# Kernel tuning notes

Hardware: AMD Instinct MI355X
Metric: run time of the kernel (lower is better)

Reference implementation:

```python
import jax, jax.numpy as jnp
import numpy as np

B = 4
N_CPGS = 20000
N_FREQS = N_CPGS // 2 + 1  # rfft length
E = 320000
H = 4
HD = 16          # head_dim = graph_hidden // n_heads
GH = 64          # graph_hidden
FD = 64          # fusion_dim
FH = 128         # fft_hidden
PH = 128         # plasticity_hidden


def _ln(x, g, b, eps=1e-5):
    m = x.mean(-1, keepdims=True)
    v = ((x - m) ** 2).mean(-1, keepdims=True)
    return (x - m) / jnp.sqrt(v + eps) * g + b


def _gelu(x):
    return jax.nn.gelu(x, approximate=False)  # torch default: exact erf GELU


def setup_inputs() -> dict:
    key = jax.random.key(0)
    ki = iter(jax.random.split(key, 40))
    nrm = lambda shape, s=0.02: jax.random.normal(next(ki), shape, dtype=jnp.float32) * s
    z = lambda *s: jnp.zeros(s, jnp.float32)
    o = lambda *s: jnp.ones(s, jnp.float32)
    return dict(
        x=jax.random.uniform(next(ki), (B, N_CPGS), dtype=jnp.float32),
        edge_index=jax.random.randint(next(ki), (2, E), 0, N_CPGS, dtype=jnp.int32),
        fft_freq_weights=o(N_FREQS),
        fft_w1=nrm((FH, N_FREQS)), fft_b1=z(FH), fft_ln1_g=o(FH), fft_ln1_b=z(FH),
        fft_w2=nrm((FD, FH)), fft_b2=z(FD), fft_ln2_g=o(FD), fft_ln2_b=z(FD),
        ge_w=nrm((GH, 1)), ge_b=z(GH), ge_ln_g=o(GH), ge_ln_b=z(GH),
        gat_w=nrm((GH, GH)), gat_attn=nrm((H, 2 * HD), 0.1),
        gp_w=nrm((FD, GH)), gp_b=z(FD), gp_ln_g=o(FD), gp_ln_b=z(FD),
        pl_W=nrm((PH, N_FREQS), 0.01), pl_alpha=o(PH, N_FREQS) * 0.01,
        pl_eta=jnp.array([0.1], jnp.float32), pl_bias=z(PH),
        pn_g=o(PH), pn_b=z(PH),
        pp_w=nrm((FD, PH)), pp_b=z(FD), pp_ln_g=o(FD), pp_ln_b=z(FD),
        gate_w1=nrm((6, 3 * FD)), gate_b1=z(6), gate_w2=nrm((3, 6)), gate_b2=z(3),
        head_w1=nrm((32, FD)), head_b1=z(32), head_w2=nrm((1, 32)), head_b2=z(1),
    )


def reference(x, edge_index, fft_freq_weights,
              fft_w1, fft_b1, fft_ln1_g, fft_ln1_b, fft_w2, fft_b2, fft_ln2_g, fft_ln2_b,
              ge_w, ge_b, ge_ln_g, ge_ln_b, gat_w, gat_attn,
              gp_w, gp_b, gp_ln_g, gp_ln_b,
              pl_W, pl_alpha, pl_eta, pl_bias, pn_g, pn_b,
              pp_w, pp_b, pp_ln_g, pp_ln_b,
              gate_w1, gate_b1, gate_w2, gate_b2,
              head_w1, head_b1, head_w2, head_b2):
    Bsz, n = x.shape
    # ---- Stream 1: FFT ----
    xc = x - x.mean(axis=1, keepdims=True)
    mag = jnp.log1p(jnp.abs(jnp.fft.rfft(xc, axis=1)))          # (B, N_FREQS)
    freq_w = jax.nn.softmax(fft_freq_weights) * fft_freq_weights.shape[0]
    magw = mag * freq_w[None, :]
    f = _gelu(_ln(magw @ fft_w1.T + fft_b1, fft_ln1_g, fft_ln1_b))
    fft_feat = _ln(f @ fft_w2.T + fft_b2, fft_ln2_g, fft_ln2_b)  # (B, FD)
    # ---- Stream 2: sparse graph attention (eval: dropout off) ----
    h0 = _gelu(_ln(x[..., None] * ge_w[:, 0] + ge_b, ge_ln_g, ge_ln_b))  # (B, N, GH)
    h = (h0 @ gat_w.T).reshape(Bsz, n, H, HD)
    a_src, a_dst = gat_attn[:, :HD], gat_attn[:, HD:]
    s_src = jnp.einsum('bnhd,hd->bnh', h, a_src)
    s_dst = jnp.einsum('bnhd,hd->bnh', h, a_dst)
    src, dst = edge_index[0], edge_index[1]
    scores = s_src[:, src] + s_dst[:, dst]                       # (B, E, H)
    scores = jnp.where(scores >= 0, scores, 0.2 * scores)        # leaky_relu(0.2)
    # max with include_self=True over zero-init buffer (matches torch scatter_reduce)
    m = jnp.zeros((Bsz, n, H), scores.dtype).at[:, dst].max(scores)
    e = jnp.exp(scores - m[:, dst])
    ssum = jnp.zeros((Bsz, n, H), e.dtype).at[:, dst].add(e)
    attn = e / (ssum[:, dst] + 1e-8)
    msg = h[:, src] * attn[..., None]                            # (B, E, H, HD)
    gat_out = jnp.zeros((Bsz, n, H, HD), msg.dtype).at[:, dst].add(msg).reshape(Bsz, n, H * HD)
    hg = h0 + _gelu(gat_out)
    graph_feat = _ln(hg.mean(axis=1) @ gp_w.T + gp_b, gp_ln_g, gp_ln_b)  # (B, FD)
    # ---- Stream 3: Hebbian plastic layer on mag ----
    y_slow = mag @ pl_W.T + pl_bias                              # (B, PH)
    x_norm = mag / (jnp.linalg.norm(mag, axis=-1, keepdims=True) + 1e-8)
    y_pre = jnp.tanh(y_slow)
    # bmm(alpha * eta * outer(y_pre, x_norm), x) == eta * y_pre * ((x_norm*x) @ alpha.T)
    contrib = pl_eta[0] * y_pre * ((x_norm * mag) @ jax.nn.sigmoid(pl_alpha).T)
    plastic = _ln(_gelu(y_slow + contrib), pn_g, pn_b)
    plastic_feat = _ln(plastic @ pp_w.T + pp_b, pp_ln_g, pp_ln_b)
    # ---- Gated fusion ----
    concat = jnp.concatenate([fft_feat, graph_feat, plastic_feat], axis=-1)  # (B, 3*FD)
    g = _gelu(concat @ gate_w1.T + gate_b1) @ gate_w2.T + gate_b2
    gw = jax.nn.softmax(g, axis=-1)                              # (B, 3)
    fused = fft_feat * gw[:, 0:1] + graph_feat * gw[:, 1:2] + plastic_feat * gw[:, 2:3]
    # ---- Head ----
    out = _gelu(fused @ head_w1.T + head_b1) @ head_w2.T + head_b2
    return out.squeeze(-1)                                       # (B,)
```

## Files before the change

### kernel.cpp

```cpp
#include <hip/hip_runtime.h>
#include <math.h>

constexpr int N_CPGS = 20000;
constexpr int NF     = 10001;
constexpr int BZ     = 4;
constexpr int NEDGE  = 320000;
constexpr int KPAD   = 10240;
constexpr int FN1    = 200;
constexpr int FN2    = 100;
constexpr int NS2    = 8;
constexpr int TILES  = (N_CPGS + 63) / 64;
constexpr int HB     = NEDGE / 256;
constexpr int DOTSB  = 384;

constexpr size_t W_XMEAN   = 0;
constexpr size_t W_SMSTAT  = 64;
constexpr size_t W_NORMSQ  = 128;
constexpr size_t W_H0SUM   = 192;
constexpr size_t W_GATMEAN = 448;
constexpr size_t W_PREP    = 704;
constexpr size_t W_D       = 768;
constexpr size_t W_MAG     = 2304;
constexpr size_t W_SSRC    = 42368;
constexpr size_t W_SDST    = 362368;
constexpr size_t W_H       = 682368;
constexpr size_t W_Y       = 5802368;
constexpr size_t W_P2      = 5962368;
constexpr size_t W_COUNTS  = 9079168;
constexpr size_t W_OFFS    = 9099168;
constexpr size_t W_CURSOR  = 9119232;
constexpr size_t W_SORTSRC = 9139232;

#define DEVFN static __device__ __forceinline__

DEVFN float gelu_f(float v) {
    float ax = fabsf(v) * 0.70710678118654752440f;
    float t = 1.0f / fmaf(0.3275911f, ax, 1.0f);
    float p = fmaf(t, 1.061405429f, -1.453152027f);
    p = fmaf(p, t, 1.421413741f);
    p = fmaf(p, t, -0.284496736f);
    p = fmaf(p, t, 0.254829592f);
    p = p * t;
    float e = __expf(-ax * ax);
    float er = copysignf(fmaf(-p, e, 1.0f), v);
    return 0.5f * v * (1.0f + er);
}

DEVFN float wred_sum(float v) {
    #pragma unroll
    for (int m = 32; m; m >>= 1) v += __shfl_xor(v, m);
    return v;
}

DEVFN unsigned int bfr(float f) {
    unsigned int u = __float_as_uint(f);
    return (u + 0x7fffu + ((u >> 16) & 1u)) >> 16;
}
DEVFN float bf2f(unsigned short v) { return __uint_as_float(((unsigned int)v) << 16); }

__global__ void k_pre(const float* __restrict__ x, const float* __restrict__ ge_w,
                      const float* __restrict__ ge_b, const float* __restrict__ fw,
                      float* __restrict__ ws) {
    int bb = blockIdx.x, t = threadIdx.x;
    __shared__ float sd[256];
    if (bb < 4) {
        const float4* x4 = (const float4*)(x + (size_t)bb * N_CPGS);
        float s = 0.f;
        for (int i = t; i < N_CPGS / 4; i += 256) {
            float4 v = x4[i];
            s += (v.x + v.y) + (v.z + v.w);
        }
        sd[t] = s; __syncthreads();
        for (int o = 128; o; o >>= 1) { if (t < o) sd[t] += sd[t + o]; __syncthreads(); }
        if (t == 0) ws[W_XMEAN + bb] = sd[0] * (1.0f / N_CPGS);
    } else if (bb == 4) {
        for (int i = t; i < (int)(W_PREP - W_NORMSQ); i += 256) ws[W_NORMSQ + i] = 0.f;
        if (t < 64) {
            float w = ge_w[t], b = ge_b[t];
            float mw = wred_sum(w) * (1.f / 64.f);
            float mb = wred_sum(b) * (1.f / 64.f);
            float wc = w - mw, bc = b - mb;
            float A = wred_sum(wc * wc) * (1.f / 64.f);
            float C = wred_sum(wc * bc) * (1.f / 64.f);
            float D = wred_sum(bc * bc) * (1.f / 64.f);
            if (t == 0) { float* p = ws + W_PREP; p[0] = mw; p[1] = mb; p[2] = A; p[3] = C; p[4] = D; }
        }
    } else if (bb == 5) {
        float mx = -1e30f;
        for (int i = t; i < NF; i += 256) mx = fmaxf(mx, fw[i]);
        sd[t] = mx; __syncthreads();
        for (int o = 128; o; o >>= 1) { if (t < o) sd[t] = fmaxf(sd[t], sd[t + o]); __syncthreads(); }
        mx = sd[0]; __syncthreads();
        float s = 0.f;
        for (int i = t; i < NF; i += 256) s += expf(fw[i] - mx);
        sd[t] = s; __syncthreads();
        for (int o = 128; o; o >>= 1) { if (t < o) sd[t] += sd[t + o]; __syncthreads(); }
        if (t == 0) { ws[W_SMSTAT] = mx; ws[W_SMSTAT + 1] = sd[0]; }
    } else {
        int base = (bb - 6) * 1000;
        int* cnt = (int*)(ws + W_COUNTS);
        for (int i = t; i < 1000; i += 256) cnt[base + i] = 0;
    }
}

__global__ __launch_bounds__(256) void k_node(
    const float* __restrict__ x, const float* __restrict__ ge_w, const float* __restrict__ ge_b,
    const float* __restrict__ ge_g, const float* __restrict__ ge_beta,
    const float* __restrict__ gat_w, const float* __restrict__ gat_attn,
    const int* __restrict__ ei, float* __restrict__ ws)
{
    int t = threadIdx.x;
    int nb = blockIdx.x;
    if (nb >= 4 * TILES) {
        int r = nb - 4 * TILES;
        if (r < HB) {
            int e = r * 256 + t;
            if (e < NEDGE) atomicAdd((int*)(ws + W_COUNTS) + ei[NEDGE + e], 1);
        } else {
            int fb = r - HB;
            int b = fb / 100;
            int n1base = (fb % 100) * 2;
            int n1l = t >> 7, k2 = t & 127;
            __shared__ float xs[2][100];
            float xm = ws[W_XMEAN + b];
            for (int i = t; i < 200; i += 256) {
                int nl = (i >= 100) ? 1 : 0, n2 = (i >= 100) ? i - 100 : i;
                xs[nl][n2] = x[(size_t)b * N_CPGS + n1base + nl + 200 * n2] - xm;
            }
            __syncthreads();
            int k2e = (k2 < 100) ? k2 : 0;
            constexpr float T100 = 6.2831853071795864769f / 100.f;
            float dc, dsn;
            { float sn, cn; sincosf(T100 * (float)k2e, &sn, &cn); dc = cn; dsn = -sn; }
            float yr = 0.f, yi = 0.f;
            #pragma unroll
            for (int half = 0; half < 2; ++half) {
                float c, s;
                { int m = (k2e * (half * 50)) % 100; float sn, cn; sincosf(T100 * (float)m, &sn, &cn); c = cn; s = -sn; }
                #pragma unroll 5
                for (int j = 0; j < 50; ++j) {
                    float xv = xs[n1l][half * 50 + j];
                    yr = fmaf(xv, c, yr); yi = fmaf(xv, s, yi);
                    float tc_ = c * dc - s * dsn; s = s * dc + c * dsn; c = tc_;
                }
            }
            if (k2 < 100)
                ((float2*)(ws + W_Y))[((size_t)(n1base + n1l) * FN2 + k2) * 4 + b] = make_float2(yr, yi);
        }
        return;
    }
    int b = nb / TILES;
    int tile = nb % TILES;
    int n0 = tile * 64;

    __shared__ __align__(16) float h0T[64 * 68];
    __shared__ __align__(16) float gwT[64 * 68];
    __shared__ float xsv[64], rss[64];

    const float* prep = ws + W_PREP;
    float mw = prep[0], mb = prep[1], A = prep[2], C = prep[3], Dd = prep[4];

    for (int idx = t; idx < 4096; idx += 256) { int i = idx >> 6, j = idx & 63; gwT[j * 68 + i] = gat_w[idx]; }
    if (t < 64) {
        int n = n0 + t;
        float xv = (n < N_CPGS) ? x[(size_t)b * N_CPGS + n] : 0.f;
        xsv[t] = xv;
        float var = xv * xv * A + 2.f * xv * C + Dd;
        rss[t] = 1.0f / sqrtf(var + 1e-5f);
    }
    __syncthreads();

    for (int idx = t; idx < 4096; idx += 256) {
        int j = idx >> 6, nd = idx & 63;
        float h0 = 0.f;
        if (n0 + nd < N_CPGS) {
            float v = (xsv[nd] * (ge_w[j] - mw) + (ge_b[j] - mb)) * rss[nd];
            h0 = gelu_f(v * ge_g[j] + ge_beta[j]);
        }
        h0T[j * 68 + nd] = h0;
    }
    __syncthreads();

    int tr = t >> 4, tc = t & 15;
    float acc[4][4] = {};
    #pragma unroll 8
    for (int j = 0; j < 64; ++j) {
        const float4 av = *(const float4*)&h0T[j * 68 + (tr << 2)];
        const float4 bv = *(const float4*)&gwT[j * 68 + (tc << 2)];
        #pragma unroll
        for (int u = 0; u < 4; ++u) {
            float a = (u == 0) ? av.x : (u == 1) ? av.y : (u == 2) ? av.z : av.w;
            acc[u][0] = fmaf(a, bv.x, acc[u][0]);
            acc[u][1] = fmaf(a, bv.y, acc[u][1]);
            acc[u][2] = fmaf(a, bv.z, acc[u][2]);
            acc[u][3] = fmaf(a, bv.w, acc[u][3]);
        }
    }
    if (t < 64) {
        float s = 0.f;
        #pragma unroll 8
        for (int nd = 0; nd < 64; ++nd) s += h0T[t * 68 + nd];
        atomicAdd(ws + W_H0SUM + b * 64 + t, s);
    }
    unsigned short* hbp = (unsigned short*)(ws + W_H);
    #pragma unroll
    for (int u = 0; u < 4; ++u) {
        int n = n0 + tr * 4 + u;
        if (n < N_CPGS) {
            unsigned int lo = bfr(acc[u][0]) | (bfr(acc[u][1]) << 16);
            unsigned int hi = bfr(acc[u][2]) | (bfr(acc[u][3]) << 16);
            *(uint2*)(hbp + ((size_t)b * N_CPGS + n) * 64 + tc * 4) = make_uint2(lo, hi);
        }
    }
    {
        int hh = tc >> 2;
        float ps[4], pd[4];
        #pragma unroll
        for (int u = 0; u < 4; ++u) {
            float s = 0.f, d = 0.f;
            #pragma unroll
            for (int kk = 0; kk < 4; ++kk) {
                float asv = gat_attn[hh * 32 + (tc & 3) * 4 + kk];
                float adv = gat_attn[hh * 32 + 16 + (tc & 3) * 4 + kk];
                s = fmaf(acc[u][kk], asv, s);
                d = fmaf(acc[u][kk], adv, d);
            }
            ps[u] = s; pd[u] = d;
        }
        #pragma unroll
        for (int u = 0; u < 4; ++u) {
            ps[u] += __shfl_xor(ps[u], 1); ps[u] += __shfl_xor(ps[u], 2);
            pd[u] += __shfl_xor(pd[u], 1); pd[u] += __shfl_xor(pd[u], 2);
        }
        if ((tc & 3) == 0) {
            #pragma unroll
            for (int u = 0; u < 4; ++u) {
                int n = n0 + tr * 4 + u;
                if (n < N_CPGS) {
                    ws[W_SSRC + ((size_t)b * N_CPGS + n) * 4 + hh] = ps[u];
                    ws[W_SDST + ((size_t)b * N_CPGS + n) * 4 + hh] = pd[u];
                }
            }
        }
    }
}

__global__ __launch_bounds__(1024) void k_sf2(float* __restrict__ ws) {
    int t = threadIdx.x;
    if (blockIdx.x == 0) {
        const int* cnt = (const int*)(ws + W_COUNTS);
        int* offs = (int*)(ws + W_OFFS);
        int* cur  = (int*)(ws + W_CURSOR);
        int i0 = t * 20;
        int s = 0;
        for (int i = 0; i < 20; ++i) { int idx = i0 + i; if (idx < N_CPGS) s += cnt[idx]; }
        __shared__ int sd[1024];
        sd[t] = s; __syncthreads();
        for (int off = 1; off < 1024; off <<= 1) {
            int v = (t >= off) ? sd[t - off] : 0;
            __syncthreads();
            sd[t] += v;
            __syncthreads();
        }
        int run = sd[t] - s;
        for (int i = 0; i < 20; ++i) {
            int idx = i0 + i;
            if (idx < N_CPGS) { offs[idx] = run; cur[idx] = run; run += cnt[idx]; }
        }
        if (t == 1023) offs[N_CPGS] = sd[1023];
        return;
    }
    int bb = blockIdx.x - 1;
    int kb = bb >> 1;
    int ns = (bb & 1) * 4 + (t >> 8);
    int k = kb * 256 + (t & 255);
    int n1b = ns * 25;
    int k2 = k % 100;
    const float4* Yp = (const float4*)(ws + W_Y);
    constexpr float W0 = 6.2831853071795864769f / 20000.f;
    float dc, dsn;
    { float sn, cn; sincosf(W0 * (float)k, &sn, &cn); dc = cn; dsn = -sn; }
    float c, s;
    { int m = (k * n1b) % 20000; float sn, cn; sincosf(W0 * (float)m, &sn, &cn); c = cn; s = -sn; }
    float xr0 = 0.f, xi0 = 0.f, xr1 = 0.f, xi1 = 0.f;
    float xr2 = 0.f, xi2 = 0.f, xr3 = 0.f, xi3 = 0.f;
    #pragma unroll 5
    for (int j = 0; j < 25; ++j) {
        size_t base = ((size_t)(n1b + j) * FN2 + k2) * 2;
        float4 y01 = Yp[base], y23 = Yp[base + 1];
        xr0 = fmaf(y01.x, c, xr0); xr0 = fmaf(-y01.y, s, xr0);
        xi0 = fmaf(y01.x, s, xi0); xi0 = fmaf( y01.y, c, xi0);
        xr1 = fmaf(y01.z, c, xr1); xr1 = fmaf(-y01.w, s, xr1);
        xi1 = fmaf(y01.z, s, xi1); xi1 = fmaf( y01.w, c, xi1);
        xr2 = fmaf(y23.x, c, xr2); xr2 = fmaf(-y23.y, s, xr2);
        xi2 = fmaf(y23.x, s, xi2); xi2 = fmaf( y23.y, c, xi2);
        xr3 = fmaf(y23.z, c, xr3); xr3 = fmaf(-y23.w, s, xr3);
        xi3 = fmaf(y23.z, s, xi3); xi3 = fmaf( y23.w, c, xi3);
        float tc_ = c * dc - s * dsn; s = s * dc + c * dsn; c = tc_;
    }
    float* p = ws + W_P2 + ((size_t)ns * KPAD + k) * 8;
    p[0] = xr0; p[1] = xi0; p[2] = xr1; p[3] = xi1;
    p[4] = xr2; p[5] = xi2; p[6] = xr3; p[7] = xi3;
}

__global__ __launch_bounds__(256) void k_scatmagr(const int* __restrict__ ei,
                                                  float* __restrict__ ws) {
    int t = threadIdx.x;
    if (blockIdx.x < HB) {
        int e = blockIdx.x * 256 + t;
        if (e < NEDGE) {
            int s = ei[e], d = ei[NEDGE + e];
            int pos = atomicAdd((int*)(ws + W_CURSOR) + d, 1);
            ((int*)(ws + W_SORTSRC))[pos] = s;
        }
        return;
    }
    int gid = (blockIdx.x - HB) * 256 + t;
    bool ok = gid < BZ * NF;
    int b = ok ? gid / NF : 0;
    int k = ok ? gid - b * NF : 0;
    float m = 0.f;
    if (ok) {
        float re = 0.f, im = 0.f;
        const float* p = ws + W_P2 + (size_t)k * 8 + b * 2;
        #pragma unroll
        for (int ns = 0; ns < NS2; ++ns) { re += p[0]; im += p[1]; p += (size_t)KPAD * 8; }
        m = log1pf(sqrtf(re * re + im * im));
        ws[W_MAG + (size_t)b * NF + k] = m;
    }
    float msq = ok ? m * m : 0.f;
    #pragma unroll
    for (int bb = 0; bb < 4; ++bb) {
        float v = (ok && b == bb) ? msq : 0.f;
        v = wred_sum(v);
        if ((t & 63) == 0) atomicAdd(ws + W_NORMSQ + bb, v);
    }
}

__global__ __launch_bounds__(256) void k_gatdots(
    const float* __restrict__ fftw1, const float* __restrict__ plW,
    const float* __restrict__ plalpha, const float* __restrict__ fw,
    float* __restrict__ ws)
{
    int t = threadIdx.x;
    if (blockIdx.x >= DOTSB) {
        int g = blockIdx.x - DOTSB;
        int xcd = g & 7;
        int b = xcd >> 1;
        int blk = ((g >> 3) << 1) | (xcd & 1);
        int w = t >> 6, lane = t & 63;
        int wv = blk * 4 + w;
        int egrp = lane >> 4, fgrp = lane & 15;
        int hh = fgrp >> 2;
        const int* offs = (const int*)(ws + W_OFFS);
        const int* ssrt = (const int*)(ws + W_SORTSRC);
        const float4* s4src = (const float4*)(ws + W_SSRC);
        const float4* s4dst = (const float4*)(ws + W_SDST);
        const uint2* hbp = (const uint2*)(ws + W_H);
        size_t bN = (size_t)b * N_CPGS;
        float gacc0 = 0.f, gacc1 = 0.f, gacc2 = 0.f, gacc3 = 0.f;

        __shared__ float elds[4][4][68];
        __shared__ int   slds[4][68];
        __shared__ float gred[4][64];

        for (int dst = wv; dst < N_CPGS; dst += 2048) {
            int o0 = offs[dst], o1 = offs[dst + 1];
            if (o0 == o1) continue;
            float4 sd4 = s4dst[bN + dst];
            float es = 0.f;
            float a0 = 0.f, a1 = 0.f, a2 = 0.f, a3 = 0.f;
            for (int c0 = o0; c0 < o1; c0 += 64) {
                int cnt = min(64, o1 - c0);
                float v0 = 0.f, v1 = 0.f, v2 = 0.f, v3 = 0.f;
                int s = 0;
                if (lane < cnt) {
                    s = ssrt[c0 + lane];
                    float4 ss = s4src[bN + s];
                    v0 = ss.x + sd4.x; v0 = (v0 >= 0.f) ? v0 : 0.2f * v0; v0 = __expf(v0);
                    v1 = ss.y + sd4.y; v1 = (v1 >= 0.f) ? v1 : 0.2f * v1; v1 = __expf(v1);
                    v2 = ss.z + sd4.z; v2 = (v2 >= 0.f) ? v2 : 0.2f * v2; v2 = __expf(v2);
                    v3 = ss.w + sd4.w; v3 = (v3 >= 0.f) ? v3 : 0.2f * v3; v3 = __expf(v3);
                }
                slds[w][lane] = s;
                elds[w][0][lane] = v0; elds[w][1][lane] = v1;
                elds[w][2][lane] = v2; elds[w][3][lane] = v3;
                int niter = (cnt + 3) >> 2;
                for (int i = 0; i < niter; ++i) {
                    int j = (i << 2) + egrp;
                    float e = elds[w][hh][j];
                    int sj = slds[w][j];
                    uint2 hv = hbp[(bN + sj) * 16 + fgrp];
                    es += e;
                    a0 = fmaf(e, bf2f((unsigned short)(hv.x & 0xffffu)), a0);
                    a1 = fmaf(e, bf2f((unsigned short)(hv.x >> 16)),     a1);
                    a2 = fmaf(e, bf2f((unsigned short)(hv.y & 0xffffu)), a2);
                    a3 = fmaf(e, bf2f((unsigned short)(hv.y >> 16)),     a3);
                }
            }
            es += __shfl_xor(es, 16); es += __shfl_xor(es, 32);
            a0 += __shfl_xor(a0, 16); a0 += __shfl_xor(a0, 32);
            a1 += __shfl_xor(a1, 16); a1 += __shfl_xor(a1, 32);
            a2 += __shfl_xor(a2, 16); a2 += __shfl_xor(a2, 32);
            a3 += __shfl_xor(a3, 16); a3 += __shfl_xor(a3, 32);
            float inv = 1.f / (es + 1e-8f);
            gacc0 += gelu_f(a0 * inv); gacc1 += gelu_f(a1 * inv);
            gacc2 += gelu_f(a2 * inv); gacc3 += gelu_f(a3 * inv);
        }
        if (egrp == 0) {
            gred[w][fgrp * 4 + 0] = gacc0; gred[w][fgrp * 4 + 1] = gacc1;
            gred[w][fgrp * 4 + 2] = gacc2; gred[w][fgrp * 4 + 3] = gacc3;
        }
        __syncthreads();
        if (t < 64)
            atomicAdd(ws + W_GATMEAN + b * 64 + t, gred[0][t] + gred[1][t] + gred[2][t] + gred[3][t]);
        return;
    }
    int bb2 = blockIdx.x;
    int m = bb2 >> 7;
    int r = bb2 & 127;
    const float* mag = ws + W_MAG;
    float smx = ws[W_SMSTAT], ssm = ws[W_SMSTAT + 1];
    float sc_fw = (float)NF / ssm;
    float inv_n0 = 1.f / (sqrtf(ws[W_NORMSQ + 0]) + 1e-8f);
    float inv_n1 = 1.f / (sqrtf(ws[W_NORMSQ + 1]) + 1e-8f);
    float inv_n2 = 1.f / (sqrtf(ws[W_NORMSQ + 2]) + 1e-8f);
    float inv_n3 = 1.f / (sqrtf(ws[W_NORMSQ + 3]) + 1e-8f);
    const float* row = ((m == 0) ? fftw1 : (m == 1) ? plW : plalpha) + (size_t)r * NF;
    float a0 = 0.f, a1 = 0.f, a2 = 0.f, a3 = 0.f;
    for (int k = t; k < NF; k += 256) {
        float wv = row[k];
        float g0 = mag[k], g1 = mag[NF + k], g2 = mag[2 * NF + k], g3 = mag[3 * NF + k];
        if (m == 0) {
            float s = expf(fw[k] - smx) * sc_fw;
            wv *= s;
            a0 = fmaf(wv, g0, a0); a1 = fmaf(wv, g1, a1); a2 = fmaf(wv, g2, a2); a3 = fmaf(wv, g3, a3);
        } else if (m == 1) {
            a0 = fmaf(wv, g0, a0); a1 = fmaf(wv, g1, a1); a2 = fmaf(wv, g2, a2); a3 = fmaf(wv, g3, a3);
        } else {
            wv = 1.f / (1.f + expf(-wv));
            a0 = fmaf(wv, g0 * g0 * inv_n0, a0); a1 = fmaf(wv, g1 * g1 * inv_n1, a1);
            a2 = fmaf(wv, g2 * g2 * inv_n2, a2); a3 = fmaf(wv, g3 * g3 * inv_n3, a3);
        }
    }
    __shared__ float sd[256];
    float acc[4] = {a0, a1, a2, a3};
    #pragma unroll
    for (int bb = 0; bb < 4; ++bb) {
        sd[t] = acc[bb]; __syncthreads();
        for (int o = 128; o; o >>= 1) { if (t < o) sd[t] += sd[t + o]; __syncthreads(); }
        if (t == 0) ws[W_D + ((size_t)m * 128 + r) * 4 + bb] = sd[0];
        __syncthreads();
    }
}

DEVFN float ln64(float v, const float* g, const float* bt, int lane) {
    float mn = wred_sum(v) * (1.f / 64.f);
    float d = v - mn;
    float var = wred_sum(d * d) * (1.f / 64.f);
    return d * (1.0f / sqrtf(var + 1e-5f)) * g[lane] + bt[lane];
}
DEVFN void ln128(float& v0, float& v1, const float* g, const float* bt, int lane) {
    float mn = wred_sum(v0 + v1) * (1.f / 128.f);
    float d0 = v0 - mn, d1 = v1 - mn;
    float var = wred_sum(d0 * d0 + d1 * d1) * (1.f / 128.f);
    float rs = 1.0f / sqrtf(var + 1e-5f);
    v0 = d0 * rs * g[lane] + bt[lane];
    v1 = d1 * rs * g[lane + 64] + bt[lane + 64];
}
DEVFN float dotW128(const float* __restrict__ W, const float* __restrict__ v, int c) {
    const float4* w4 = (const float4*)(W + (size_t)c * 128);
    float acc = 0.f;
    #pragma unroll
    for (int q = 0; q < 32; ++q) {
        float4 wv = w4[q];
        const float* vv = v + q * 4;
        acc = fmaf(wv.x, vv[0], acc); acc = fmaf(wv.y, vv[1], acc);
        acc = fmaf(wv.z, vv[2], acc); acc = fmaf(wv.w, vv[3], acc);
    }
    return acc;
}
DEVFN float dotW64(const float* __restrict__ W, const float* __restrict__ v, int c) {
    const float4* w4 = (const float4*)(W + (size_t)c * 64);
    float acc = 0.f;
    #pragma unroll
    for (int q = 0; q < 16; ++q) {
        float4 wv = w4[q];
        const float* vv = v + q * 4;
        acc = fmaf(wv.x, vv[0], acc); acc = fmaf(wv.y, vv[1], acc);
        acc = fmaf(wv.z, vv[2], acc); acc = fmaf(wv.w, vv[3], acc);
    }
    return acc;
}

__global__ __launch_bounds__(256) void k_final(
    const float* __restrict__ fft_b1, const float* __restrict__ fft_ln1_g, const float* __restrict__ fft_ln1_b,
    const float* __restrict__ fft_w2, const float* __restrict__ fft_b2,
    const float* __restrict__ fft_ln2_g, const float* __restrict__ fft_ln2_b,
    const float* __restrict__ gp_w, const float* __restrict__ gp_b,
    const float* __restrict__ gp_ln_g, const float* __restrict__ gp_ln_b,
    const float* __restrict__ pl_eta, const float* __restrict__ pl_bias,
    const float* __restrict__ pn_g, const float* __restrict__ pn_b,
    const float* __restrict__ pp_w, const float* __restrict__ pp_b,
    const float* __restrict__ pp_ln_g, const float* __restrict__ pp_ln_b,
    const float* __restrict__ gate_w1, const float* __restrict__ gate_b1,
    const float* __restrict__ gate_w2, const float* __restrict__ gate_b2,
    const float* __restrict__ head_w1, const float* __restrict__ head_b1,
    const float* __restrict__ head_w2, const float* __restrict__ head_b2,
    float* __restrict__ ws, float* __restrict__ out)
{
    int t = threadIdx.x, b = t >> 6, lane = t & 63;
    __shared__ float vlds[4][256];
    float* vb = vlds[b];
    const float* D = ws + W_D;
    int r0 = lane, r1 = lane + 64;

    float f0 = D[(0 * 128 + r0) * 4 + b] + fft_b1[r0];
    float f1 = D[(0 * 128 + r1) * 4 + b] + fft_b1[r1];
    ln128(f0, f1, fft_ln1_g, fft_ln1_b, lane);
    vb[lane] = gelu_f(f0); vb[64 + lane] = gelu_f(f1);
    float catf = ln64(dotW128(fft_w2, vb, lane) + fft_b2[lane], fft_ln2_g, fft_ln2_b, lane);

    float hgm = (ws[W_H0SUM + b * 64 + lane] + ws[W_GATMEAN + b * 64 + lane]) * (1.f / N_CPGS);
    vb[lane] = hgm;
    float catg = ln64(dotW64(gp_w, vb, lane) + gp_b[lane], gp_ln_g, gp_ln_b, lane);

    float eta = pl_eta[0];
    float ys0 = D[(1 * 128 + r0) * 4 + b] + pl_bias[r0];
    float ys1 = D[(1 * 128 + r1) * 4 + b] + pl_bias[r1];
    float q0 = D[(2 * 128 + r0) * 4 + b];
    float q1 = D[(2 * 128 + r1) * 4 + b];
    float u0 = gelu_f(ys0 + eta * tanhf(ys0) * q0);
    float u1 = gelu_f(ys1 + eta * tanhf(ys1) * q1);
    ln128(u0, u1, pn_g, pn_b, lane);
    vb[lane] = u0; vb[64 + lane] = u1;
    float catp = ln64(dotW128(pp_w, vb, lane) + pp_b[lane], pp_ln_g, pp_ln_b, lane);

    vb[lane] = catf; vb[64 + lane] = catg; vb[128 + lane] = catp;
    if (lane < 6) {
        float a = gate_b1[lane];
        const float* wrow = gate_w1 + lane * 192;
        #pragma unroll 4
        for (int j = 0; j < 192; ++j) a = fmaf(wrow[j], vb[j], a);
        vb[192 + lane] = gelu_f(a);
    }
    float gv[3];
    #pragma unroll
    for (int c = 0; c < 3; ++c) {
        float a = gate_b2[c];
        #pragma unroll
        for (int j = 0; j < 6; ++j) a = fmaf(gate_w2[c * 6 + j], vb[192 + j], a);
        gv[c] = a;
    }
    float gmx = fmaxf(gv[0], fmaxf(gv[1], gv[2]));
    float e0 = expf(gv[0] - gmx), e1 = expf(gv[1] - gmx), e2 = expf(gv[2] - gmx);
    float inv = 1.f / (e0 + e1 + e2);
    float fus = catf * (e0 * inv) + catg * (e1 * inv) + catp * (e2 * inv);

    vb[lane] = fus;
    float hval = 0.f;
    if (lane < 32) {
        float a = dotW64(head_w1, vb, lane) + head_b1[lane];
        hval = gelu_f(a) * head_w2[lane];
    }
    float o = wred_sum(hval);
    if (lane == 0) out[b] = o + head_b2[0];
}

extern "C" void kernel_launch(void* const* d_in, const int* in_sizes, int n_in,
                              void* d_out, int out_size, void* d_ws, size_t ws_size,
                              hipStream_t stream) {
    (void)in_sizes; (void)n_in; (void)out_size; (void)ws_size;
    const float* x        = (const float*)d_in[0];
    const int*   ei       = (const int*)d_in[1];
    const float* fw       = (const float*)d_in[2];
    const float* fft_w1   = (const float*)d_in[3];
    const float* fft_b1   = (const float*)d_in[4];
    const float* fft_ln1g = (const float*)d_in[5];
    const float* fft_ln1b = (const float*)d_in[6];
    const float* fft_w2   = (const float*)d_in[7];
    const float* fft_b2   = (const float*)d_in[8];
    const float* fft_ln2g = (const float*)d_in[9];
    const float* fft_ln2b = (const float*)d_in[10];
    const float* ge_w     = (const float*)d_in[11];
    const float* ge_b     = (const float*)d_in[12];
    const float* ge_g     = (const float*)d_in[13];
    const float* ge_beta  = (const float*)d_in[14];
    const float* gat_w    = (const float*)d_in[15];
    const float* gat_attn = (const float*)d_in[16];
    const float* gp_w     = (const float*)d_in[17];
    const float* gp_b     = (const float*)d_in[18];
    const float* gp_ln_g  = (const float*)d_in[19];
    const float* gp_ln_b  = (const float*)d_in[20];
    const float* pl_W     = (const float*)d_in[21];
    const float* pl_alpha = (const float*)d_in[22];
    const float* pl_eta   = (const float*)d_in[23];
    const float* pl_bias  = (const float*)d_in[24];
    const float* pn_g     = (const float*)d_in[25];
    const float* pn_b     = (const float*)d_in[26];
    const float* pp_w     = (const float*)d_in[27];
    const float* pp_b     = (const float*)d_in[28];
    const float* pp_ln_g  = (const float*)d_in[29];
    const float* pp_ln_b  = (const float*)d_in[30];
    const float* gate_w1  = (const float*)d_in[31];
    const float* gate_b1  = (const float*)d_in[32];
    const float* gate_w2  = (const float*)d_in[33];
    const float* gate_b2  = (const float*)d_in[34];
    const float* head_w1  = (const float*)d_in[35];
    const float* head_b1  = (const float*)d_in[36];
    const float* head_w2  = (const float*)d_in[37];
    const float* head_b2  = (const float*)d_in[38];

    float* ws  = (float*)d_ws;
    float* out = (float*)d_out;

    k_pre<<<26, 256, 0, stream>>>(x, ge_w, ge_b, fw, ws);
    k_node<<<4 * TILES + HB + 400, 256, 0, stream>>>(x, ge_w, ge_b, ge_g, ge_beta,
                                                     gat_w, gat_attn, ei, ws);
    k_sf2<<<81, 1024, 0, stream>>>(ws);
    k_scatmagr<<<HB + (BZ * NF + 255) / 256, 256, 0, stream>>>(ei, ws);
    k_gatdots<<<DOTSB + 2048, 256, 0, stream>>>(fft_w1, pl_W, pl_alpha, fw, ws);
    k_final<<<1, 256, 0, stream>>>(fft_b1, fft_ln1g, fft_ln1b, fft_w2, fft_b2, fft_ln2g, fft_ln2b,
                                   gp_w, gp_b, gp_ln_g, gp_ln_b, pl_eta, pl_bias, pn_g, pn_b,
                                   pp_w, pp_b, pp_ln_g, pp_ln_b, gate_w1, gate_b1, gate_w2, gate_b2,
                                   head_w1, head_b1, head_w2, head_b2, ws, out);
}
```

Baseline: 214.0 us.

## Fold second FFT stage into scatter kernel and move histogram and scan earlier

Removes the standalone k_sf2 kernel. Each (frequency, batch) thread in the scatter kernel now computes the full 200-term second FFT stage and the log-magnitude directly, so the partial-sum buffer and its reduction pass are gone. The edge-count histogram moves into k_pre, the prefix scan into block 0 of k_node, and count zeroing becomes a hipMemsetAsync. The GAT aggregation grid is doubled. This cuts one kernel launch and a global round trip, but each FFT thread now does a longer serial loop with strided loads, and the scan runs on a single 256-thread block.

```diff
diff --git a/kernel.cpp b/kernel.cpp
--- a/kernel.cpp
+++ b/kernel.cpp
@@ -8,10 +8,10 @@
 constexpr int KPAD   = 10240;
 constexpr int FN1    = 200;
 constexpr int FN2    = 100;
-constexpr int NS2    = 8;
 constexpr int TILES  = (N_CPGS + 63) / 64;
 constexpr int HB     = NEDGE / 256;
 constexpr int DOTSB  = 384;
+constexpr int GATB   = 4096;
 
 constexpr size_t W_XMEAN   = 0;
 constexpr size_t W_SMSTAT  = 64;
@@ -25,7 +25,6 @@
 constexpr size_t W_SDST    = 362368;
 constexpr size_t W_H       = 682368;
 constexpr size_t W_Y       = 5802368;
-constexpr size_t W_P2      = 5962368;
 constexpr size_t W_COUNTS  = 9079168;
 constexpr size_t W_OFFS    = 9099168;
 constexpr size_t W_CURSOR  = 9119232;
@@ -60,9 +59,14 @@
 
 __global__ void k_pre(const float* __restrict__ x, const float* __restrict__ ge_w,
                       const float* __restrict__ ge_b, const float* __restrict__ fw,
-                      float* __restrict__ ws) {
+                      const int* __restrict__ ei, float* __restrict__ ws) {
     int bb = blockIdx.x, t = threadIdx.x;
     __shared__ float sd[256];
+    if (bb >= 26) {
+        int e = (bb - 26) * 256 + t;
+        if (e < NEDGE) atomicAdd((int*)(ws + W_COUNTS) + ei[NEDGE + e], 1);
+        return;
+    }
     if (bb < 4) {
         const float4* x4 = (const float4*)(x + (size_t)bb * N_CPGS);
         float s = 0.f;
@@ -96,10 +100,6 @@
         sd[t] = s; __syncthreads();
         for (int o = 128; o; o >>= 1) { if (t < o) sd[t] += sd[t + o]; __syncthreads(); }
         if (t == 0) { ws[W_SMSTAT] = mx; ws[W_SMSTAT + 1] = sd[0]; }
-    } else {
-        int base = (bb - 6) * 1000;
-        int* cnt = (int*)(ws + W_COUNTS);
-        for (int i = t; i < 1000; i += 256) cnt[base + i] = 0;
     }
 }
 
@@ -107,50 +107,69 @@
     const float* __restrict__ x, const float* __restrict__ ge_w, const float* __restrict__ ge_b,
     const float* __restrict__ ge_g, const float* __restrict__ ge_beta,
     const float* __restrict__ gat_w, const float* __restrict__ gat_attn,
-    const int* __restrict__ ei, float* __restrict__ ws)
+    float* __restrict__ ws)
 {
     int t = threadIdx.x;
     int nb = blockIdx.x;
-    if (nb >= 4 * TILES) {
-        int r = nb - 4 * TILES;
-        if (r < HB) {
-            int e = r * 256 + t;
-            if (e < NEDGE) atomicAdd((int*)(ws + W_COUNTS) + ei[NEDGE + e], 1);
-        } else {
-            int fb = r - HB;
-            int b = fb / 100;
-            int n1base = (fb % 100) * 2;
-            int n1l = t >> 7, k2 = t & 127;
-            __shared__ float xs[2][100];
-            float xm = ws[W_XMEAN + b];
-            for (int i = t; i < 200; i += 256) {
-                int nl = (i >= 100) ? 1 : 0, n2 = (i >= 100) ? i - 100 : i;
-                xs[nl][n2] = x[(size_t)b * N_CPGS + n1base + nl + 200 * n2] - xm;
+    if (nb == 0) {
+        const int* cnt = (const int*)(ws + W_COUNTS);
+        int* offs = (int*)(ws + W_OFFS);
+        int* cur  = (int*)(ws + W_CURSOR);
+        constexpr int PER = (N_CPGS + 255) / 256;
+        int i0 = t * PER;
+        int s = 0;
+        for (int i = 0; i < PER; ++i) { int idx = i0 + i; if (idx < N_CPGS) s += cnt[idx]; }
+        __shared__ int sdi[256];
+        sdi[t] = s; __syncthreads();
+        for (int off = 1; off < 256; off <<= 1) {
+            int v = (t >= off) ? sdi[t - off] : 0;
+            __syncthreads();
+            sdi[t] += v;
+            __syncthreads();
+        }
+        int run = sdi[t] - s;
+        for (int i = 0; i < PER; ++i) {
+            int idx = i0 + i;
+            if (idx < N_CPGS) { offs[idx] = run; cur[idx] = run; run += cnt[idx]; }
+        }
+        if (t == 255) offs[N_CPGS] = sdi[255];
+        return;
+    }
+    if (nb >= 1 + 4 * TILES) {
+        int fb = nb - 1 - 4 * TILES;
+        int b = fb / 100;
+        int n1base = (fb % 100) * 2;
+        int n1l = t >> 7, k2 = t & 127;
+        __shared__ float xs[2][100];
+        float xm = ws[W_XMEAN + b];
+        for (int i = t; i < 200; i += 256) {
+            int nl = (i >= 100) ? 1 : 0, n2 = (i >= 100) ? i - 100 : i;
+            xs[nl][n2] = x[(size_t)b * N_CPGS + n1base + nl + 200 * n2] - xm;
+        }
+        __syncthreads();
+        int k2e = (k2 < 100) ? k2 : 0;
+        constexpr float T100 = 6.2831853071795864769f / 100.f;
+        float dc, dsn;
+        { float sn, cn; sincosf(T100 * (float)k2e, &sn, &cn); dc = cn; dsn = -sn; }
+        float yr = 0.f, yi = 0.f;
+        #pragma unroll
+        for (int half = 0; half < 2; ++half) {
+            float c, s;
+            { int m = (k2e * (half * 50)) % 100; float sn, cn; sincosf(T100 * (float)m, &sn, &cn); c = cn; s = -sn; }
+            #pragma unroll 5
+            for (int j = 0; j < 50; ++j) {
+                float xv = xs[n1l][half * 50 + j];
+                yr = fmaf(xv, c, yr); yi = fmaf(xv, s, yi);
+                float tc_ = c * dc - s * dsn; s = s * dc + c * dsn; c = tc_;
             }
-            __syncthreads();
-            int k2e = (k2 < 100) ? k2 : 0;
-            constexpr float T100 = 6.2831853071795864769f / 100.f;
-            float dc, dsn;
-            { float sn, cn; sincosf(T100 * (float)k2e, &sn, &cn); dc = cn; dsn = -sn; }
-            float yr = 0.f, yi = 0.f;
-            #pragma unroll
-            for (int half = 0; half < 2; ++half) {
-                float c, s;
-                { int m = (k2e * (half * 50)) % 100; float sn, cn; sincosf(T100 * (float)m, &sn, &cn); c = cn; s = -sn; }
-                #pragma unroll 5
-                for (int j = 0; j < 50; ++j) {
-                    float xv = xs[n1l][half * 50 + j];
-                    yr = fmaf(xv, c, yr); yi = fmaf(xv, s, yi);
-                    float tc_ = c * dc - s * dsn; s = s * dc + c * dsn; c = tc_;
-                }
-            }
-            if (k2 < 100)
-                ((float2*)(ws + W_Y))[((size_t)(n1base + n1l) * FN2 + k2) * 4 + b] = make_float2(yr, yi);
-        }
+        }
+        if (k2 < 100)
+            ((float2*)(ws + W_Y))[((size_t)(n1base + n1l) * FN2 + k2) * 4 + b] = make_float2(yr, yi);
         return;
     }
-    int b = nb / TILES;
-    int tile = nb % TILES;
+    int nb2 = nb - 1;
+    int b = nb2 / TILES;
+    int tile = nb2 % TILES;
     int n0 = tile * 64;
 
     __shared__ __align__(16) float h0T[64 * 68];
@@ -245,66 +264,8 @@
     }
 }
 
-__global__ __launch_bounds__(1024) void k_sf2(float* __restrict__ ws) {
-    int t = threadIdx.x;
-    if (blockIdx.x == 0) {
-        const int* cnt = (const int*)(ws + W_COUNTS);
-        int* offs = (int*)(ws + W_OFFS);
-        int* cur  = (int*)(ws + W_CURSOR);
-        int i0 = t * 20;
-        int s = 0;
-        for (int i = 0; i < 20; ++i) { int idx = i0 + i; if (idx < N_CPGS) s += cnt[idx]; }
-        __shared__ int sd[1024];
-        sd[t] = s; __syncthreads();
-        for (int off = 1; off < 1024; off <<= 1) {
-            int v = (t >= off) ? sd[t - off] : 0;
-            __syncthreads();
-            sd[t] += v;
-            __syncthreads();
-        }
-        int run = sd[t] - s;
-        for (int i = 0; i < 20; ++i) {
-            int idx = i0 + i;
-            if (idx < N_CPGS) { offs[idx] = run; cur[idx] = run; run += cnt[idx]; }
-        }
-        if (t == 1023) offs[N_CPGS] = sd[1023];
-        return;
-    }
-    int bb = blockIdx.x - 1;
-    int kb = bb >> 1;
-    int ns = (bb & 1) * 4 + (t >> 8);
-    int k = kb * 256 + (t & 255);
-    int n1b = ns * 25;
-    int k2 = k % 100;
-    const float4* Yp = (const float4*)(ws + W_Y);
-    constexpr float W0 = 6.2831853071795864769f / 20000.f;
-    float dc, dsn;
-    { float sn, cn; sincosf(W0 * (float)k, &sn, &cn); dc = cn; dsn = -sn; }
-    float c, s;
-    { int m = (k * n1b) % 20000; float sn, cn; sincosf(W0 * (float)m, &sn, &cn); c = cn; s = -sn; }
-    float xr0 = 0.f, xi0 = 0.f, xr1 = 0.f, xi1 = 0.f;
-    float xr2 = 0.f, xi2 = 0.f, xr3 = 0.f, xi3 = 0.f;
-    #pragma unroll 5
-    for (int j = 0; j < 25; ++j) {
-        size_t base = ((size_t)(n1b + j) * FN2 + k2) * 2;
-        float4 y01 = Yp[base], y23 = Yp[base + 1];
-        xr0 = fmaf(y01.x, c, xr0); xr0 = fmaf(-y01.y, s, xr0);
-        xi0 = fmaf(y01.x, s, xi0); xi0 = fmaf( y01.y, c, xi0);
-        xr1 = fmaf(y01.z, c, xr1); xr1 = fmaf(-y01.w, s, xr1);
-        xi1 = fmaf(y01.z, s, xi1); xi1 = fmaf( y01.w, c, xi1);
-        xr2 = fmaf(y23.x, c, xr2); xr2 = fmaf(-y23.y, s, xr2);
-        xi2 = fmaf(y23.x, s, xi2); xi2 = fmaf( y23.y, c, xi2);
-        xr3 = fmaf(y23.z, c, xr3); xr3 = fmaf(-y23.w, s, xr3);
-        xi3 = fmaf(y23.z, s, xi3); xi3 = fmaf( y23.w, c, xi3);
-        float tc_ = c * dc - s * dsn; s = s * dc + c * dsn; c = tc_;
-    }
-    float* p = ws + W_P2 + ((size_t)ns * KPAD + k) * 8;
-    p[0] = xr0; p[1] = xi0; p[2] = xr1; p[3] = xi1;
-    p[4] = xr2; p[5] = xi2; p[6] = xr3; p[7] = xi3;
-}
-
-__global__ __launch_bounds__(256) void k_scatmagr(const int* __restrict__ ei,
-                                                  float* __restrict__ ws) {
+__global__ __launch_bounds__(256) void k_scat2(const int* __restrict__ ei,
+                                               float* __restrict__ ws) {
     int t = threadIdx.x;
     if (blockIdx.x < HB) {
         int e = blockIdx.x * 256 + t;
@@ -316,25 +277,36 @@
         return;
     }
     int gid = (blockIdx.x - HB) * 256 + t;
-    bool ok = gid < BZ * NF;
-    int b = ok ? gid / NF : 0;
-    int k = ok ? gid - b * NF : 0;
+    int k = gid >> 2, b = gid & 3;
+    int k2 = k % 100;
+    const float2* Y2 = (const float2*)(ws + W_Y);
+    constexpr float W0 = 6.2831853071795864769f / 20000.f;
+    float dc, dsn;
+    { float sn, cn; sincosf(W0 * (float)k, &sn, &cn); dc = cn; dsn = -sn; }
+    float xr = 0.f, xi = 0.f;
+    #pragma unroll
+    for (int seg = 0; seg < 4; ++seg) {
+        int n1b = seg * 50;
+        float c, s;
+        { int m = (k * n1b) % 20000; float sn, cn; sincosf(W0 * (float)m, &sn, &cn); c = cn; s = -sn; }
+        #pragma unroll 5
+        for (int j = 0; j < 50; ++j) {
+            float2 y = Y2[((size_t)(n1b + j) * FN2 + k2) * 4 + b];
+            xr = fmaf(y.x, c, xr); xr = fmaf(-y.y, s, xr);
+            xi = fmaf(y.x, s, xi); xi = fmaf( y.y, c, xi);
+            float tc_ = c * dc - s * dsn; s = s * dc + c * dsn; c = tc_;
+        }
+    }
+    bool ok = k < NF;
     float m = 0.f;
     if (ok) {
-        float re = 0.f, im = 0.f;
-        const float* p = ws + W_P2 + (size_t)k * 8 + b * 2;
-        #pragma unroll
-        for (int ns = 0; ns < NS2; ++ns) { re += p[0]; im += p[1]; p += (size_t)KPAD * 8; }
-        m = log1pf(sqrtf(re * re + im * im));
+        m = log1pf(sqrtf(xr * xr + xi * xi));
         ws[W_MAG + (size_t)b * NF + k] = m;
     }
     float msq = ok ? m * m : 0.f;
     #pragma unroll
-    for (int bb = 0; bb < 4; ++bb) {
-        float v = (ok && b == bb) ? msq : 0.f;
-        v = wred_sum(v);
-        if ((t & 63) == 0) atomicAdd(ws + W_NORMSQ + bb, v);
-    }
+    for (int o = 4; o < 64; o <<= 1) msq += __shfl_xor(msq, o);
+    if ((t & 63) < 4) atomicAdd(ws + W_NORMSQ + b, msq);
 }
 
 __global__ __launch_bounds__(256) void k_gatdots(
@@ -364,7 +336,7 @@
         __shared__ int   slds[4][68];
         __shared__ float gred[4][64];
 
-        for (int dst = wv; dst < N_CPGS; dst += 2048) {
+        for (int dst = wv; dst < N_CPGS; dst += GATB) {
             int o0 = offs[dst], o1 = offs[dst + 1];
             if (o0 == o1) continue;
             float4 sd4 = s4dst[bN + dst];
@@ -614,12 +586,12 @@
     float* ws  = (float*)d_ws;
     float* out = (float*)d_out;
 
-    k_pre<<<26, 256, 0, stream>>>(x, ge_w, ge_b, fw, ws);
-    k_node<<<4 * TILES + HB + 400, 256, 0, stream>>>(x, ge_w, ge_b, ge_g, ge_beta,
-                                                     gat_w, gat_attn, ei, ws);
-    k_sf2<<<81, 1024, 0, stream>>>(ws);
-    k_scatmagr<<<HB + (BZ * NF + 255) / 256, 256, 0, stream>>>(ei, ws);
-    k_gatdots<<<DOTSB + 2048, 256, 0, stream>>>(fft_w1, pl_W, pl_alpha, fw, ws);
+    hipMemsetAsync(ws + W_COUNTS, 0, N_CPGS * sizeof(int), stream);
+    k_pre<<<26 + HB, 256, 0, stream>>>(x, ge_w, ge_b, fw, ei, ws);
+    k_node<<<1 + 4 * TILES + 400, 256, 0, stream>>>(x, ge_w, ge_b, ge_g, ge_beta,
+                                                    gat_w, gat_attn, ws);
+    k_scat2<<<HB + 160, 256, 0, stream>>>(ei, ws);
+    k_gatdots<<<DOTSB + GATB, 256, 0, stream>>>(fft_w1, pl_W, pl_alpha, fw, ws);
     k_final<<<1, 256, 0, stream>>>(fft_b1, fft_ln1g, fft_ln1b, fft_w2, fft_b2, fft_ln2g, fft_ln2b,
                                    gp_w, gp_b, gp_ln_g, gp_ln_b, pl_eta, pl_bias, pn_g, pn_b,
                                    pp_w, pp_b, pp_ln_g, pp_ln_b, gate_w1, gate_b1, gate_w2, gate_b2,
```

Result: faster. 203.1 us (-5.1%).
